# Kernel optimization log

Measured on AMD Instinct MI355X. Metric: run time of the kernel, lower is better.

## Reference

```python
import jax, jax.numpy as jnp
import numpy as np

N, E, H, ED = 20000, 640000, 128, 16


def _lin_init(k, fan_in, fan_out):
    kw, kb = jax.random.split(k)
    lim = 1.0 / np.sqrt(fan_in)
    W = jax.random.uniform(kw, (fan_in, fan_out), jnp.float32, -lim, lim)
    b = jax.random.uniform(kb, (fan_out,), jnp.float32, -lim, lim)
    return W, b


def setup_inputs() -> dict:
    key = jax.random.key(0)
    ks = jax.random.split(key, 12)
    h = jax.random.normal(ks[0], (N, H), jnp.float32)
    x = jax.random.normal(ks[1], (N, 3), jnp.float32)
    edge_index = jax.random.randint(ks[2], (2, E), 0, N, jnp.int32)
    edge_attr = jax.random.normal(ks[3], (E, ED), jnp.float32)
    fixed_mask = jax.random.randint(ks[4], (N,), 0, 2, jnp.int32).astype(bool)
    We1, be1 = _lin_init(ks[5], 2 * H + 1 + ED, H)
    We2, be2 = _lin_init(ks[6], H, H)
    Wx1, bx1 = _lin_init(ks[7], H, H)
    Wx2, bx2 = _lin_init(ks[8], H, 1)
    Wh1, bh1 = _lin_init(ks[9], 2 * H, H)
    Wh2, bh2 = _lin_init(ks[10], H, H)
    return {"h": h, "x": x, "edge_index": edge_index, "edge_attr": edge_attr,
            "fixed_mask": fixed_mask,
            "We1": We1, "be1": be1, "We2": We2, "be2": be2,
            "Wx1": Wx1, "bx1": bx1, "Wx2": Wx2, "bx2": bx2,
            "Wh1": Wh1, "bh1": bh1, "Wh2": Wh2, "bh2": bh2}


def reference(h, x, edge_index, edge_attr, fixed_mask,
              We1, be1, We2, be2, Wx1, bx1, Wx2, bx2, Wh1, bh1, Wh2, bh2):
    src, dst = edge_index[0], edge_index[1]
    n = h.shape[0]
    diff = x[src] - x[dst]                               # [E,3]
    dist_sq_norm = jnp.sum(diff * diff, -1, keepdims=True) / 100.0
    e_in = jnp.concatenate([h[src], h[dst], dist_sq_norm, edge_attr], -1)
    m_ij = jax.nn.silu(jax.nn.silu(e_in @ We1 + be1) @ We2 + be2)  # [E,H]
    coord_w = jnp.tanh(jax.nn.silu(m_ij @ Wx1 + bx1) @ Wx2 + bx2)  # [E,1]
    coord_agg = jax.ops.segment_sum(diff * coord_w, dst, num_segments=n)
    coord_agg = coord_agg * (~fixed_mask).astype(h.dtype)[:, None]
    msg_agg = jax.ops.segment_sum(m_ij, dst, num_segments=n)       # [N,H]
    h_new = h + jax.nn.silu(jnp.concatenate([h, msg_agg], -1) @ Wh1 + bh1) @ Wh2 + bh2
    x_new = x + coord_agg
    return h_new, x_new
```

## Files before the change

kernel.cpp:

```cpp
#include <hip/hip_runtime.h>
#include <hip/hip_bf16.h>
#include <math.h>

#define NN   20000
#define NE   640000
#define HD   128
#define EDIM 16
#define KIN  273
#define P2   136

#define S_PWT   4096
#define S_PWE1M 32768
#define S_PW4   16384
#define S_PWH1  32768
#define S_PWH2  16384

typedef __bf16 bf16x8 __attribute__((ext_vector_type(8)));
typedef float  f32x4  __attribute__((ext_vector_type(4)));

__device__ __forceinline__ float silu_f(float v) {
    const float e = __expf(-v);
    return v * __builtin_amdgcn_rcpf(1.0f + e);
}
__device__ __forceinline__ float tanh_f(float s) {
    const float e = __expf(2.0f * s);
    return 1.0f - 2.0f * __builtin_amdgcn_rcpf(e + 1.0f);
}
__device__ __forceinline__ unsigned short f2bf(float f) {
    __bf16 b = (__bf16)f;
    return __builtin_bit_cast(unsigned short, b);
}
__device__ __forceinline__ float bf2f(unsigned short u) {
    __bf16 b = __builtin_bit_cast(__bf16, u);
    return (float)b;
}
__device__ __forceinline__ unsigned pack2bf(float a, float b) {
    return (unsigned)f2bf(a) | ((unsigned)f2bf(b) << 16);
}

__device__ __forceinline__ void pack_id(const float* __restrict__ W, int Kreal,
                                        unsigned short* __restrict__ P, int idx) {
    const int f = idx >> 9, r = idx & 511;
    const int lane = r >> 3, j = r & 7;
    const int kb = f >> 3, nb = f & 7;
    const int k = kb * 32 + (lane >> 4) * 8 + j;
    const int n = nb * 16 + (lane & 15);
    P[idx] = f2bf((k < Kreal) ? W[(size_t)k * HD + n] : 0.0f);
}
__device__ __forceinline__ void pack_il(const float* __restrict__ W, int Kreal,
                                        unsigned short* __restrict__ P, int idx) {
    const int f = idx >> 9, r = idx & 511;
    const int lane = r >> 3, j = r & 7;
    const int kb = f >> 3, nb = f & 7;
    const int k = kb * 32 + (lane >> 4) * 8 + j;
    const int n = (nb >> 1) * 32 + 2 * (lane & 15) + (nb & 1);
    P[idx] = f2bf((k < Kreal) ? W[(size_t)k * HD + n] : 0.0f);
}

#define ZDW (NN*(HD+3))

__global__ void egnn_prep_kernel(
    const float* __restrict__ h, const int* __restrict__ ei,
    const float* __restrict__ We1, const float* __restrict__ We2,
    const float* __restrict__ Wx1, const float* __restrict__ Wh1,
    const float* __restrict__ Wh2,
    int* __restrict__ zbase,
    unsigned short* __restrict__ hb,
    unsigned short* __restrict__ PWt,  unsigned short* __restrict__ PWe1m,
    unsigned short* __restrict__ PWe2, unsigned short* __restrict__ PWx1,
    unsigned short* __restrict__ PWh1, unsigned short* __restrict__ PWh2,
    int* __restrict__ cnt)
{
    const size_t NH4 = (size_t)NN * HD / 4;
    const size_t Z1 = ZDW, C1 = Z1 + NH4;
    const size_t T1 = C1 + S_PWT, T2 = T1 + S_PWE1M, T3 = T2 + S_PW4;
    const size_t T4 = T3 + S_PW4, T5 = T4 + S_PWH1, T6 = T5 + S_PWH2;
    const size_t TOT = T6 + NE;
    const size_t stride = (size_t)gridDim.x * blockDim.x;
    for (size_t i = (size_t)blockIdx.x * blockDim.x + threadIdx.x; i < TOT; i += stride) {
        if (i < Z1) { zbase[i] = 0; continue; }
        if (i < C1) {
            const size_t r = i - Z1;
            const float4 v = ((const float4*)h)[r];
            unsigned* dst = (unsigned*)&hb[r * 4];
            dst[0] = pack2bf(v.x, v.y);
            dst[1] = pack2bf(v.z, v.w);
            continue;
        }
        if (i < T1) {
            const int idx = (int)(i - C1);
            const int r = idx & 511, nb = idx >> 9;
            const int lane = r >> 3, j = r & 7;
            const int k = 256 + (lane >> 4) * 8 + j;
            const int n = (nb >> 1) * 32 + 2 * (lane & 15) + (nb & 1);
            PWt[idx] = f2bf((k < KIN) ? We1[(size_t)k * HD + n] : 0.0f);
            continue;
        }
        if (i < T2) { pack_il(We1, 256, PWe1m, (int)(i - T1)); continue; }
        if (i < T3) { pack_il(We2, HD, PWe2, (int)(i - T2)); continue; }
        if (i < T4) { pack_il(Wx1, HD, PWx1, (int)(i - T3)); continue; }
        if (i < T5) { pack_id(Wh1, 2 * HD, PWh1, (int)(i - T4)); continue; }
        if (i < T6) { pack_id(Wh2, HD, PWh2, (int)(i - T5)); continue; }
        atomicAdd(&cnt[ei[NE + (i - T6)]], 1);
    }
}

__global__ __launch_bounds__(256, 4) void egnn_pre_kernel(
    const unsigned short* __restrict__ hb,
    const unsigned short* __restrict__ PWe1m, const float* __restrict__ be1,
    const int* __restrict__ cnt, int* __restrict__ cursor,
    unsigned short* __restrict__ preS, unsigned short* __restrict__ preD)
{
    const int t = threadIdx.x;
    if (blockIdx.x == 313) {
        __shared__ int ls[256];
        const int base = t * 79;
        int c[79];
        int s = 0;
        for (int i = 0; i < 79; ++i) {
            const int idx = base + i;
            c[i] = (idx < NN) ? cnt[idx] : 0;
            s += c[i];
        }
        ls[t] = s;
        __syncthreads();
        int v = s;
        for (int off = 1; off < 256; off <<= 1) {
            const int u = (t >= off) ? ls[t - off] : 0;
            __syncthreads();
            v += u;
            ls[t] = v;
            __syncthreads();
        }
        int run = v - s;
        for (int i = 0; i < 79; ++i) {
            const int idx = base + i;
            if (idx < NN) { cursor[idx] = run; run += c[i]; }
        }
        return;
    }
    const int n0 = blockIdx.x * 64;
    const int lane = t & 63, w = t >> 6;
    const int quad = lane >> 4, l16 = lane & 15;
    int arow[4];
    #pragma unroll
    for (int mb = 0; mb < 4; ++mb) arow[mb] = min(n0 + mb * 16 + l16, NN - 1);

    f32x4 accS[4][2], accD[4][2];
    #pragma unroll
    for (int mb = 0; mb < 4; ++mb)
        #pragma unroll
        for (int nt = 0; nt < 2; ++nt) {
            accS[mb][nt] = (f32x4){0.f,0.f,0.f,0.f};
            accD[mb][nt] = (f32x4){0.f,0.f,0.f,0.f};
        }
    #pragma unroll
    for (int kb = 0; kb < 4; ++kb) {
        bf16x8 a[4], bS[2], bD[2];
        #pragma unroll
        for (int mb = 0; mb < 4; ++mb)
            a[mb] = *(const bf16x8*)&hb[(size_t)arow[mb] * HD + kb * 32 + quad * 8];
        #pragma unroll
        for (int nt = 0; nt < 2; ++nt) {
            bS[nt] = *(const bf16x8*)&PWe1m[((kb * 8 + w * 2 + nt) * 64 + lane) * 8];
            bD[nt] = *(const bf16x8*)&PWe1m[(((4 + kb) * 8 + w * 2 + nt) * 64 + lane) * 8];
        }
        #pragma unroll
        for (int mb = 0; mb < 4; ++mb)
            #pragma unroll
            for (int nt = 0; nt < 2; ++nt) {
                accS[mb][nt] = __builtin_amdgcn_mfma_f32_16x16x32_bf16(
                    a[mb], bS[nt], accS[mb][nt], 0, 0, 0);
                accD[mb][nt] = __builtin_amdgcn_mfma_f32_16x16x32_bf16(
                    a[mb], bD[nt], accD[mb][nt], 0, 0, 0);
            }
    }
    const int cb = w * 32 + 2 * l16;
    const float2 b1 = *(const float2*)&be1[cb];
    #pragma unroll
    for (int mb = 0; mb < 4; ++mb)
        #pragma unroll
        for (int r = 0; r < 4; ++r) {
            const int n = n0 + mb * 16 + quad * 4 + r;
            if (n < NN) {
                *(unsigned*)&preS[(size_t)n * HD + cb] =
                    pack2bf(accS[mb][0][r], accS[mb][1][r]);
                *(unsigned*)&preD[(size_t)n * HD + cb] =
                    pack2bf(accD[mb][0][r] + b1.x, accD[mb][1][r] + b1.y);
            }
        }
}

__global__ void egnn_perm_kernel(const int* __restrict__ ei,
                                 int* __restrict__ cursor, int* __restrict__ perm) {
    const int e = blockIdx.x * 256 + threadIdx.x;
    const int pos = atomicAdd(&cursor[ei[NE + e]], 1);
    perm[pos] = e;
}

__global__ __launch_bounds__(256, 6) void egnn_edge_kernel(
    const unsigned short* __restrict__ preS, const unsigned short* __restrict__ preD,
    const float* __restrict__ x,
    const int* __restrict__ ei, const float* __restrict__ eattr,
    const int* __restrict__ perm,
    const unsigned short* __restrict__ PWt,
    const unsigned short* __restrict__ PWe2, const float* __restrict__ be2,
    const unsigned short* __restrict__ PWx1, const float* __restrict__ bx1,
    const float* __restrict__ Wx2, const float* __restrict__ bx2,
    float* __restrict__ msg_agg, float* __restrict__ coord_agg)
{
    __shared__ __align__(16) unsigned short buf[64 * P2];
    __shared__ int   sE[64], sSrc[64], sDst[64];
    __shared__ float sDiff[64][3];
    __shared__ float sW[64];

    const int t  = threadIdx.x;
    const int e0 = blockIdx.x * 64;
    unsigned short* tail = buf;

    if (t < 64) {
        const int e = perm[e0 + t];
        sE[t] = e;
        const int s = ei[e];
        const int d = ei[NE + e];
        sSrc[t] = s; sDst[t] = d;
        const float dx = x[s*3+0] - x[d*3+0];
        const float dy = x[s*3+1] - x[d*3+1];
        const float dz = x[s*3+2] - x[d*3+2];
        sDiff[t][0] = dx; sDiff[t][1] = dy; sDiff[t][2] = dz;
        tail[t * 32 + 0] = f2bf((dx*dx + dy*dy + dz*dz) * 0.01f);
    }
    __syncthreads();

    const int lane = t & 63;
    const int w    = t >> 6;
    const int quad = lane >> 4;
    const int l16  = lane & 15;
    const int cb   = w * 32 + 2 * l16;

    f32x4 preC[4][2];
    #pragma unroll
    for (int mb = 0; mb < 4; ++mb)
        #pragma unroll
        for (int r = 0; r < 4; ++r) {
            const int row = mb * 16 + quad * 4 + r;
            const unsigned us = *(const unsigned*)&preS[(size_t)sSrc[row] * HD + cb];
            const unsigned ud = *(const unsigned*)&preD[(size_t)sDst[row] * HD + cb];
            preC[mb][0][r] = bf2f((unsigned short)(us & 0xffff)) +
                             bf2f((unsigned short)(ud & 0xffff));
            preC[mb][1][r] = bf2f((unsigned short)(us >> 16)) +
                             bf2f((unsigned short)(ud >> 16));
        }

    {
        const int eL = t >> 2, q = t & 3;
        const int eG = sE[eL];
        #pragma unroll
        for (int jj = 0; jj < 8; ++jj) {
            const int col = q * 8 + jj;
            if (col == 0) continue;
            float v = 0.0f;
            if (col <= EDIM) v = eattr[(size_t)eG * EDIM + (col - 1)];
            tail[eL * 32 + col] = f2bf(v);
        }
    }
    __syncthreads();

    f32x4 acc1[4][2];
    {
        bf16x8 a[4], b[2];
        #pragma unroll
        for (int mb = 0; mb < 4; ++mb)
            a[mb] = *(const bf16x8*)&tail[(mb * 16 + l16) * 32 + quad * 8];
        #pragma unroll
        for (int nt = 0; nt < 2; ++nt)
            b[nt] = *(const bf16x8*)&PWt[((w * 2 + nt) * 64 + lane) * 8];
        #pragma unroll
        for (int mb = 0; mb < 4; ++mb)
            #pragma unroll
            for (int nt = 0; nt < 2; ++nt)
                acc1[mb][nt] = __builtin_amdgcn_mfma_f32_16x16x32_bf16(
                    a[mb], b[nt], preC[mb][nt], 0, 0, 0);
    }
    __syncthreads();

    #pragma unroll
    for (int mb = 0; mb < 4; ++mb)
        #pragma unroll
        for (int r = 0; r < 4; ++r) {
            const int row = mb * 16 + quad * 4 + r;
            *(unsigned*)&buf[row * P2 + cb] =
                pack2bf(silu_f(acc1[mb][0][r]), silu_f(acc1[mb][1][r]));
        }
    __syncthreads();

    f32x4 acc2[4][2];
    #pragma unroll
    for (int mb = 0; mb < 4; ++mb)
        #pragma unroll
        for (int nt = 0; nt < 2; ++nt) acc2[mb][nt] = (f32x4){0.f,0.f,0.f,0.f};
    #pragma unroll
    for (int kb = 0; kb < 4; ++kb) {
        bf16x8 a[4], b[2];
        #pragma unroll
        for (int mb = 0; mb < 4; ++mb)
            a[mb] = *(const bf16x8*)&buf[(mb * 16 + l16) * P2 + kb * 32 + quad * 8];
        #pragma unroll
        for (int nt = 0; nt < 2; ++nt)
            b[nt] = *(const bf16x8*)&PWe2[((kb * 8 + w * 2 + nt) * 64 + lane) * 8];
        #pragma unroll
        for (int mb = 0; mb < 4; ++mb)
            #pragma unroll
            for (int nt = 0; nt < 2; ++nt)
                acc2[mb][nt] = __builtin_amdgcn_mfma_f32_16x16x32_bf16(
                    a[mb], b[nt], acc2[mb][nt], 0, 0, 0);
    }
    __syncthreads();

    {
        const float2 b2 = *(const float2*)&be2[cb];
        #pragma unroll
        for (int mb = 0; mb < 4; ++mb)
            #pragma unroll
            for (int r = 0; r < 4; ++r) {
                const int row = mb * 16 + quad * 4 + r;
                *(unsigned*)&buf[row * P2 + cb] =
                    pack2bf(silu_f(acc2[mb][0][r] + b2.x),
                            silu_f(acc2[mb][1][r] + b2.y));
            }
    }
    __syncthreads();

    {
        const int cp = t & 63;
        const int r0 = (t >> 6) * 16;
        float a0 = 0.0f, a1 = 0.0f;
        #pragma unroll 4
        for (int r = 0; r < 16; ++r) {
            const int row = r0 + r;
            const int d   = sDst[row];
            const unsigned u = *(const unsigned*)&buf[row * P2 + 2 * cp];
            a0 += bf2f((unsigned short)(u & 0xffff));
            a1 += bf2f((unsigned short)(u >> 16));
            const bool flush = (r == 15) || (sDst[row + 1] != d);
            if (flush) {
                atomicAdd(&msg_agg[(size_t)d * HD + 2 * cp], a0);
                atomicAdd(&msg_agg[(size_t)d * HD + 2 * cp + 1], a1);
                a0 = 0.0f; a1 = 0.0f;
            }
        }
    }

    f32x4 acc3[4][2];
    #pragma unroll
    for (int mb = 0; mb < 4; ++mb)
        #pragma unroll
        for (int nt = 0; nt < 2; ++nt) acc3[mb][nt] = (f32x4){0.f,0.f,0.f,0.f};
    #pragma unroll
    for (int kb = 0; kb < 4; ++kb) {
        bf16x8 a[4], b[2];
        #pragma unroll
        for (int mb = 0; mb < 4; ++mb)
            a[mb] = *(const bf16x8*)&buf[(mb * 16 + l16) * P2 + kb * 32 + quad * 8];
        #pragma unroll
        for (int nt = 0; nt < 2; ++nt)
            b[nt] = *(const bf16x8*)&PWx1[((kb * 8 + w * 2 + nt) * 64 + lane) * 8];
        #pragma unroll
        for (int mb = 0; mb < 4; ++mb)
            #pragma unroll
            for (int nt = 0; nt < 2; ++nt)
                acc3[mb][nt] = __builtin_amdgcn_mfma_f32_16x16x32_bf16(
                    a[mb], b[nt], acc3[mb][nt], 0, 0, 0);
    }
    float p[4][4];
    {
        const float2 bx = *(const float2*)&bx1[cb];
        const float2 w2 = *(const float2*)&Wx2[cb];
        #pragma unroll
        for (int mb = 0; mb < 4; ++mb)
            #pragma unroll
            for (int r = 0; r < 4; ++r)
                p[mb][r] = silu_f(acc3[mb][0][r] + bx.x) * w2.x +
                           silu_f(acc3[mb][1][r] + bx.y) * w2.y;
        #pragma unroll
        for (int off = 8; off >= 1; off >>= 1)
            #pragma unroll
            for (int mb = 0; mb < 4; ++mb)
                #pragma unroll
                for (int r = 0; r < 4; ++r)
                    p[mb][r] += __shfl_xor(p[mb][r], off, 64);
    }
    __syncthreads();

    if (l16 == 0) {
        float* red = reinterpret_cast<float*>(buf);
        #pragma unroll
        for (int mb = 0; mb < 4; ++mb)
            #pragma unroll
            for (int r = 0; r < 4; ++r)
                red[w * 64 + mb * 16 + quad * 4 + r] = p[mb][r];
    }
    __syncthreads();
    if (t < 64) {
        const float* red = reinterpret_cast<const float*>(buf);
        sW[t] = tanh_f(red[t] + red[64 + t] + red[128 + t] + red[192 + t] + bx2[0]);
    }
    __syncthreads();

    if (w < 3) {
        const int dstv = sDst[lane];
        float v = sDiff[lane][w] * sW[lane];
        #pragma unroll
        for (int off = 1; off <= 32; off <<= 1) {
            const int   dn = __shfl_down(dstv, off, 64);
            const float vn = __shfl_down(v, off, 64);
            if (lane + off < 64 && dn == dstv) v += vn;
        }
        const int up = __shfl_up(dstv, 1, 64);
        if (lane == 0 || up != dstv)
            atomicAdd(&coord_agg[(size_t)dstv * 3 + w], v);
    }
}

__global__ __launch_bounds__(256, 4) void egnn_node_kernel(
    const unsigned short* __restrict__ hb, const float* __restrict__ h,
    const float* __restrict__ x, const int* __restrict__ fixed_mask,
    const unsigned short* __restrict__ PWh1, const float* __restrict__ bh1,
    const unsigned short* __restrict__ PWh2, const float* __restrict__ bh2,
    const float* __restrict__ msg_agg, const float* __restrict__ coord_agg,
    float* __restrict__ out_h, float* __restrict__ out_x)
{
    __shared__ __align__(16) unsigned short sTn[64 * P2];
    const int t  = threadIdx.x;
    const int n0 = blockIdx.x * 64;
    const int lane = t & 63, w = t >> 6;
    const int quad = lane >> 4, l16 = lane & 15;

    if (t < 192) {
        const int ln = t / 3, d3 = t - ln * 3;
        const int n  = n0 + ln;
        if (n < NN) {
            const float add = (fixed_mask[n] != 0) ? 0.0f : coord_agg[(size_t)n*3 + d3];
            out_x[(size_t)n*3 + d3] = x[(size_t)n*3 + d3] + add;
        }
    }

    int nrow[4];
    #pragma unroll
    for (int mb = 0; mb < 4; ++mb) nrow[mb] = min(n0 + mb * 16 + l16, NN - 1);

    f32x4 acc[4][2];
    #pragma unroll
    for (int mb = 0; mb < 4; ++mb)
        #pragma unroll
        for (int nt = 0; nt < 2; ++nt) acc[mb][nt] = (f32x4){0.f,0.f,0.f,0.f};

    #pragma unroll
    for (int kb = 0; kb < 8; ++kb) {
        bf16x8 a[4], b[2];
        if (kb < 4) {
            #pragma unroll
            for (int mb = 0; mb < 4; ++mb)
                a[mb] = *(const bf16x8*)&hb[(size_t)nrow[mb] * HD + kb * 32 + quad * 8];
        } else {
            #pragma unroll
            for (int mb = 0; mb < 4; ++mb) {
                const float* mp = msg_agg + (size_t)nrow[mb] * HD + (kb - 4) * 32 + quad * 8;
                const float4 v0 = ((const float4*)mp)[0];
                const float4 v1 = ((const float4*)mp)[1];
                bf16x8 av;
                av[0]=(__bf16)v0.x; av[1]=(__bf16)v0.y; av[2]=(__bf16)v0.z; av[3]=(__bf16)v0.w;
                av[4]=(__bf16)v1.x; av[5]=(__bf16)v1.y; av[6]=(__bf16)v1.z; av[7]=(__bf16)v1.w;
                a[mb] = av;
            }
        }
        #pragma unroll
        for (int nt = 0; nt < 2; ++nt)
            b[nt] = *(const bf16x8*)&PWh1[((kb * 8 + w * 2 + nt) * 64 + lane) * 8];
        #pragma unroll
        for (int mb = 0; mb < 4; ++mb)
            #pragma unroll
            for (int nt = 0; nt < 2; ++nt)
                acc[mb][nt] = __builtin_amdgcn_mfma_f32_16x16x32_bf16(
                    a[mb], b[nt], acc[mb][nt], 0, 0, 0);
    }
    #pragma unroll
    for (int nt = 0; nt < 2; ++nt) {
        const int col = w * 32 + nt * 16 + l16;
        const float bias = bh1[col];
        #pragma unroll
        for (int mb = 0; mb < 4; ++mb)
            #pragma unroll
            for (int r = 0; r < 4; ++r) {
                const int row = mb * 16 + quad * 4 + r;
                sTn[row * P2 + col] = f2bf(silu_f(acc[mb][nt][r] + bias));
            }
    }
    __syncthreads();

    #pragma unroll
    for (int mb = 0; mb < 4; ++mb)
        #pragma unroll
        for (int nt = 0; nt < 2; ++nt) acc[mb][nt] = (f32x4){0.f,0.f,0.f,0.f};
    #pragma unroll
    for (int kb = 0; kb < 4; ++kb) {
        bf16x8 a[4], b[2];
        #pragma unroll
        for (int mb = 0; mb < 4; ++mb)
            a[mb] = *(const bf16x8*)&sTn[(mb * 16 + l16) * P2 + kb * 32 + quad * 8];
        #pragma unroll
        for (int nt = 0; nt < 2; ++nt)
            b[nt] = *(const bf16x8*)&PWh2[((kb * 8 + w * 2 + nt) * 64 + lane) * 8];
        #pragma unroll
        for (int mb = 0; mb < 4; ++mb)
            #pragma unroll
            for (int nt = 0; nt < 2; ++nt)
                acc[mb][nt] = __builtin_amdgcn_mfma_f32_16x16x32_bf16(
                    a[mb], b[nt], acc[mb][nt], 0, 0, 0);
    }
    #pragma unroll
    for (int nt = 0; nt < 2; ++nt) {
        const int col = w * 32 + nt * 16 + l16;
        const float bias = bh2[col];
        #pragma unroll
        for (int mb = 0; mb < 4; ++mb)
            #pragma unroll
            for (int r = 0; r < 4; ++r) {
                const int row = mb * 16 + quad * 4 + r;
                const int n   = n0 + row;
                if (n < NN)
                    out_h[(size_t)n * HD + col] =
                        h[(size_t)n * HD + col] + acc[mb][nt][r] + bias;
            }
    }
}

extern "C" void kernel_launch(void* const* d_in, const int* in_sizes, int n_in,
                              void* d_out, int out_size, void* d_ws, size_t ws_size,
                              hipStream_t stream)
{
    const float* h     = (const float*)d_in[0];
    const float* x     = (const float*)d_in[1];
    const int*   ei    = (const int*)d_in[2];
    const float* eattr = (const float*)d_in[3];
    const int*   fmask = (const int*)d_in[4];
    const float* We1   = (const float*)d_in[5];
    const float* be1   = (const float*)d_in[6];
    const float* We2   = (const float*)d_in[7];
    const float* be2   = (const float*)d_in[8];
    const float* Wx1   = (const float*)d_in[9];
    const float* bx1   = (const float*)d_in[10];
    const float* Wx2   = (const float*)d_in[11];
    const float* bx2   = (const float*)d_in[12];
    const float* Wh1   = (const float*)d_in[13];
    const float* bh1   = (const float*)d_in[14];
    const float* Wh2   = (const float*)d_in[15];
    const float* bh2   = (const float*)d_in[16];

    float* msg    = (float*)d_ws;
    float* coord  = msg + (size_t)NN * HD;
    int*   cnt    = (int*)(coord + (size_t)NN * 3);
    int*   cursor = cnt + NN;
    int*   perm   = cursor + NN;
    unsigned short* hb    = (unsigned short*)(perm + NE);
    unsigned short* preS  = hb + (size_t)NN * HD;
    unsigned short* preD  = preS + (size_t)NN * HD;
    unsigned short* PWt   = preD + (size_t)NN * HD;
    unsigned short* PWe1m = PWt + S_PWT;
    unsigned short* PWe2  = PWe1m + S_PWE1M;
    unsigned short* PWx1  = PWe2 + S_PW4;
    unsigned short* PWh1  = PWx1 + S_PW4;
    unsigned short* PWh2  = PWh1 + S_PWH1;

    float* out_h = (float*)d_out;
    float* out_x = out_h + (size_t)NN * HD;

    hipMemsetAsync(cnt, 0, (size_t)NN * sizeof(int), stream);
    egnn_prep_kernel<<<1024, 256, 0, stream>>>(
        h, ei, We1, We2, Wx1, Wh1, Wh2, (int*)d_ws,
        hb, PWt, PWe1m, PWe2, PWx1, PWh1, PWh2, cnt);
    egnn_pre_kernel<<<314, 256, 0, stream>>>(hb, PWe1m, be1, cnt, cursor, preS, preD);
    egnn_perm_kernel<<<NE / 256, 256, 0, stream>>>(ei, cursor, perm);
    egnn_edge_kernel<<<NE / 64, 256, 0, stream>>>(
        preS, preD, x, ei, eattr, perm, PWt, PWe2, be2, PWx1, bx1,
        Wx2, bx2, msg, coord);
    egnn_node_kernel<<<(NN + 63) / 64, 256, 0, stream>>>(
        hb, h, x, fmask, PWh1, bh1, PWh2, bh2, msg, coord, out_h, out_x);
}
```

Before: 379.5 us.

## Split edge MLP MFMA work by rows per wave with interleaved weight packing

Each wave now owns 16 edge rows across all 128 output columns, where before it owned 32 columns across all 64 rows. Weights are repacked so each lane holds 8 contiguous columns, which enables 16-byte gathers of preS/preD and uint4 stores to LDS. It also removes the cross-wave LDS reduction and one barrier in the coord-weight head. In exchange each wave now loads all B fragments (8 per k-block) instead of 2, which shifts traffic from A-fragment LDS reads to weight reads.

```diff
diff --git a/kernel.cpp b/kernel.cpp
--- a/kernel.cpp
+++ b/kernel.cpp
@@ -37,6 +37,8 @@
 __device__ __forceinline__ unsigned pack2bf(float a, float b) {
     return (unsigned)f2bf(a) | ((unsigned)f2bf(b) << 16);
 }
+__device__ __forceinline__ float lo16(unsigned u) { return bf2f((unsigned short)(u & 0xffff)); }
+__device__ __forceinline__ float hi16(unsigned u) { return bf2f((unsigned short)(u >> 16)); }
 
 __device__ __forceinline__ void pack_id(const float* __restrict__ W, int Kreal,
                                         unsigned short* __restrict__ P, int idx) {
@@ -54,6 +56,15 @@
     const int kb = f >> 3, nb = f & 7;
     const int k = kb * 32 + (lane >> 4) * 8 + j;
     const int n = (nb >> 1) * 32 + 2 * (lane & 15) + (nb & 1);
+    P[idx] = f2bf((k < Kreal) ? W[(size_t)k * HD + n] : 0.0f);
+}
+__device__ __forceinline__ void pack_i8(const float* __restrict__ W, int Kreal,
+                                        unsigned short* __restrict__ P, int idx) {
+    const int f = idx >> 9, r = idx & 511;
+    const int lane = r >> 3, j = r & 7;
+    const int kb = f >> 3, nb = f & 7;
+    const int k = kb * 32 + (lane >> 4) * 8 + j;
+    const int n = 8 * (lane & 15) + nb;
     P[idx] = f2bf((k < Kreal) ? W[(size_t)k * HD + n] : 0.0f);
 }
 
@@ -92,13 +103,13 @@
             const int r = idx & 511, nb = idx >> 9;
             const int lane = r >> 3, j = r & 7;
             const int k = 256 + (lane >> 4) * 8 + j;
-            const int n = (nb >> 1) * 32 + 2 * (lane & 15) + (nb & 1);
+            const int n = 8 * (lane & 15) + nb;
             PWt[idx] = f2bf((k < KIN) ? We1[(size_t)k * HD + n] : 0.0f);
             continue;
         }
         if (i < T2) { pack_il(We1, 256, PWe1m, (int)(i - T1)); continue; }
-        if (i < T3) { pack_il(We2, HD, PWe2, (int)(i - T2)); continue; }
-        if (i < T4) { pack_il(Wx1, HD, PWx1, (int)(i - T3)); continue; }
+        if (i < T3) { pack_i8(We2, HD, PWe2, (int)(i - T2)); continue; }
+        if (i < T4) { pack_i8(Wx1, HD, PWx1, (int)(i - T3)); continue; }
         if (i < T5) { pack_id(Wh1, 2 * HD, PWh1, (int)(i - T4)); continue; }
         if (i < T6) { pack_id(Wh2, HD, PWh2, (int)(i - T5)); continue; }
         atomicAdd(&cnt[ei[NE + (i - T6)]], 1);
@@ -236,21 +247,22 @@
     const int w    = t >> 6;
     const int quad = lane >> 4;
     const int l16  = lane & 15;
-    const int cb   = w * 32 + 2 * l16;
-
-    f32x4 preC[4][2];
-    #pragma unroll
-    for (int mb = 0; mb < 4; ++mb)
-        #pragma unroll
-        for (int r = 0; r < 4; ++r) {
-            const int row = mb * 16 + quad * 4 + r;
-            const unsigned us = *(const unsigned*)&preS[(size_t)sSrc[row] * HD + cb];
-            const unsigned ud = *(const unsigned*)&preD[(size_t)sDst[row] * HD + cb];
-            preC[mb][0][r] = bf2f((unsigned short)(us & 0xffff)) +
-                             bf2f((unsigned short)(ud & 0xffff));
-            preC[mb][1][r] = bf2f((unsigned short)(us >> 16)) +
-                             bf2f((unsigned short)(ud >> 16));
-        }
+    const int c8   = 8 * l16;
+    int rowg[4];
+    #pragma unroll
+    for (int r = 0; r < 4; ++r) rowg[r] = w * 16 + quad * 4 + r;
+
+    f32x4 acc[8];
+    #pragma unroll
+    for (int r = 0; r < 4; ++r) {
+        const int row = rowg[r];
+        const uint4 us = *(const uint4*)&preS[(size_t)sSrc[row] * HD + c8];
+        const uint4 ud = *(const uint4*)&preD[(size_t)sDst[row] * HD + c8];
+        acc[0][r] = lo16(us.x) + lo16(ud.x);  acc[1][r] = hi16(us.x) + hi16(ud.x);
+        acc[2][r] = lo16(us.y) + lo16(ud.y);  acc[3][r] = hi16(us.y) + hi16(ud.y);
+        acc[4][r] = lo16(us.z) + lo16(ud.z);  acc[5][r] = hi16(us.z) + hi16(ud.z);
+        acc[6][r] = lo16(us.w) + lo16(ud.w);  acc[7][r] = hi16(us.w) + hi16(ud.w);
+    }
 
     {
         const int eL = t >> 2, q = t & 3;
@@ -266,68 +278,52 @@
     }
     __syncthreads();
 
-    f32x4 acc1[4][2];
     {
-        bf16x8 a[4], b[2];
-        #pragma unroll
-        for (int mb = 0; mb < 4; ++mb)
-            a[mb] = *(const bf16x8*)&tail[(mb * 16 + l16) * 32 + quad * 8];
-        #pragma unroll
-        for (int nt = 0; nt < 2; ++nt)
-            b[nt] = *(const bf16x8*)&PWt[((w * 2 + nt) * 64 + lane) * 8];
-        #pragma unroll
-        for (int mb = 0; mb < 4; ++mb)
-            #pragma unroll
-            for (int nt = 0; nt < 2; ++nt)
-                acc1[mb][nt] = __builtin_amdgcn_mfma_f32_16x16x32_bf16(
-                    a[mb], b[nt], preC[mb][nt], 0, 0, 0);
-    }
-    __syncthreads();
-
-    #pragma unroll
-    for (int mb = 0; mb < 4; ++mb)
+        const bf16x8 a = *(const bf16x8*)&tail[(w * 16 + l16) * 32 + quad * 8];
+        #pragma unroll
+        for (int nt = 0; nt < 8; ++nt) {
+            const bf16x8 b = *(const bf16x8*)&PWt[(nt * 64 + lane) * 8];
+            acc[nt] = __builtin_amdgcn_mfma_f32_16x16x32_bf16(a, b, acc[nt], 0, 0, 0);
+        }
+    }
+    __syncthreads();
+
+    #pragma unroll
+    for (int r = 0; r < 4; ++r) {
+        uint4 o;
+        o.x = pack2bf(silu_f(acc[0][r]), silu_f(acc[1][r]));
+        o.y = pack2bf(silu_f(acc[2][r]), silu_f(acc[3][r]));
+        o.z = pack2bf(silu_f(acc[4][r]), silu_f(acc[5][r]));
+        o.w = pack2bf(silu_f(acc[6][r]), silu_f(acc[7][r]));
+        *(uint4*)&buf[rowg[r] * P2 + c8] = o;
+    }
+    __syncthreads();
+
+    #pragma unroll
+    for (int nt = 0; nt < 8; ++nt) acc[nt] = (f32x4){0.f,0.f,0.f,0.f};
+    #pragma unroll
+    for (int kb = 0; kb < 4; ++kb) {
+        const bf16x8 a = *(const bf16x8*)&buf[(w * 16 + l16) * P2 + kb * 32 + quad * 8];
+        #pragma unroll
+        for (int nt = 0; nt < 8; ++nt) {
+            const bf16x8 b = *(const bf16x8*)&PWe2[((kb * 8 + nt) * 64 + lane) * 8];
+            acc[nt] = __builtin_amdgcn_mfma_f32_16x16x32_bf16(a, b, acc[nt], 0, 0, 0);
+        }
+    }
+    __syncthreads();
+
+    {
+        const float4 ba = *(const float4*)&be2[c8];
+        const float4 bb = *(const float4*)&be2[c8 + 4];
         #pragma unroll
         for (int r = 0; r < 4; ++r) {
-            const int row = mb * 16 + quad * 4 + r;
-            *(unsigned*)&buf[row * P2 + cb] =
-                pack2bf(silu_f(acc1[mb][0][r]), silu_f(acc1[mb][1][r]));
-        }
-    __syncthreads();
-
-    f32x4 acc2[4][2];
-    #pragma unroll
-    for (int mb = 0; mb < 4; ++mb)
-        #pragma unroll
-        for (int nt = 0; nt < 2; ++nt) acc2[mb][nt] = (f32x4){0.f,0.f,0.f,0.f};
-    #pragma unroll
-    for (int kb = 0; kb < 4; ++kb) {
-        bf16x8 a[4], b[2];
-        #pragma unroll
-        for (int mb = 0; mb < 4; ++mb)
-            a[mb] = *(const bf16x8*)&buf[(mb * 16 + l16) * P2 + kb * 32 + quad * 8];
-        #pragma unroll
-        for (int nt = 0; nt < 2; ++nt)
-            b[nt] = *(const bf16x8*)&PWe2[((kb * 8 + w * 2 + nt) * 64 + lane) * 8];
-        #pragma unroll
-        for (int mb = 0; mb < 4; ++mb)
-            #pragma unroll
-            for (int nt = 0; nt < 2; ++nt)
-                acc2[mb][nt] = __builtin_amdgcn_mfma_f32_16x16x32_bf16(
-                    a[mb], b[nt], acc2[mb][nt], 0, 0, 0);
-    }
-    __syncthreads();
-
-    {
-        const float2 b2 = *(const float2*)&be2[cb];
-        #pragma unroll
-        for (int mb = 0; mb < 4; ++mb)
-            #pragma unroll
-            for (int r = 0; r < 4; ++r) {
-                const int row = mb * 16 + quad * 4 + r;
-                *(unsigned*)&buf[row * P2 + cb] =
-                    pack2bf(silu_f(acc2[mb][0][r] + b2.x),
-                            silu_f(acc2[mb][1][r] + b2.y));
-            }
+            uint4 o;
+            o.x = pack2bf(silu_f(acc[0][r] + ba.x), silu_f(acc[1][r] + ba.y));
+            o.y = pack2bf(silu_f(acc[2][r] + ba.z), silu_f(acc[3][r] + ba.w));
+            o.z = pack2bf(silu_f(acc[4][r] + bb.x), silu_f(acc[5][r] + bb.y));
+            o.w = pack2bf(silu_f(acc[6][r] + bb.z), silu_f(acc[7][r] + bb.w));
+            *(uint4*)&buf[rowg[r] * P2 + c8] = o;
+        }
     }
     __syncthreads();
 
@@ -340,8 +336,8 @@
             const int row = r0 + r;
             const int d   = sDst[row];
             const unsigned u = *(const unsigned*)&buf[row * P2 + 2 * cp];
-            a0 += bf2f((unsigned short)(u & 0xffff));
-            a1 += bf2f((unsigned short)(u >> 16));
+            a0 += lo16(u);
+            a1 += hi16(u);
             const bool flush = (r == 15) || (sDst[row + 1] != d);
             if (flush) {
                 atomicAdd(&msg_agg[(size_t)d * HD + 2 * cp], a0);
@@ -351,59 +347,40 @@
         }
     }
 
-    f32x4 acc3[4][2];
-    #pragma unroll
-    for (int mb = 0; mb < 4; ++mb)
-        #pragma unroll
-        for (int nt = 0; nt < 2; ++nt) acc3[mb][nt] = (f32x4){0.f,0.f,0.f,0.f};
+    #pragma unroll
+    for (int nt = 0; nt < 8; ++nt) acc[nt] = (f32x4){0.f,0.f,0.f,0.f};
     #pragma unroll
     for (int kb = 0; kb < 4; ++kb) {
-        bf16x8 a[4], b[2];
-        #pragma unroll
-        for (int mb = 0; mb < 4; ++mb)
-            a[mb] = *(const bf16x8*)&buf[(mb * 16 + l16) * P2 + kb * 32 + quad * 8];
-        #pragma unroll
-        for (int nt = 0; nt < 2; ++nt)
-            b[nt] = *(const bf16x8*)&PWx1[((kb * 8 + w * 2 + nt) * 64 + lane) * 8];
-        #pragma unroll
-        for (int mb = 0; mb < 4; ++mb)
-            #pragma unroll
-            for (int nt = 0; nt < 2; ++nt)
-                acc3[mb][nt] = __builtin_amdgcn_mfma_f32_16x16x32_bf16(
-                    a[mb], b[nt], acc3[mb][nt], 0, 0, 0);
-    }
-    float p[4][4];
+        const bf16x8 a = *(const bf16x8*)&buf[(w * 16 + l16) * P2 + kb * 32 + quad * 8];
+        #pragma unroll
+        for (int nt = 0; nt < 8; ++nt) {
+            const bf16x8 b = *(const bf16x8*)&PWx1[((kb * 8 + nt) * 64 + lane) * 8];
+            acc[nt] = __builtin_amdgcn_mfma_f32_16x16x32_bf16(a, b, acc[nt], 0, 0, 0);
+        }
+    }
     {
-        const float2 bx = *(const float2*)&bx1[cb];
-        const float2 w2 = *(const float2*)&Wx2[cb];
-        #pragma unroll
-        for (int mb = 0; mb < 4; ++mb)
+        const float4 ba = *(const float4*)&bx1[c8];
+        const float4 bb = *(const float4*)&bx1[c8 + 4];
+        const float4 wa = *(const float4*)&Wx2[c8];
+        const float4 wb = *(const float4*)&Wx2[c8 + 4];
+        float p[4];
+        #pragma unroll
+        for (int r = 0; r < 4; ++r) {
+            p[r] = silu_f(acc[0][r] + ba.x) * wa.x + silu_f(acc[1][r] + ba.y) * wa.y
+                 + silu_f(acc[2][r] + ba.z) * wa.z + silu_f(acc[3][r] + ba.w) * wa.w
+                 + silu_f(acc[4][r] + bb.x) * wb.x + silu_f(acc[5][r] + bb.y) * wb.y
+                 + silu_f(acc[6][r] + bb.z) * wb.z + silu_f(acc[7][r] + bb.w) * wb.w;
+        }
+        #pragma unroll
+        for (int off = 8; off >= 1; off >>= 1)
             #pragma unroll
             for (int r = 0; r < 4; ++r)
-                p[mb][r] = silu_f(acc3[mb][0][r] + bx.x) * w2.x +
-                           silu_f(acc3[mb][1][r] + bx.y) * w2.y;
-        #pragma unroll
-        for (int off = 8; off >= 1; off >>= 1)
-            #pragma unroll
-            for (int mb = 0; mb < 4; ++mb)
-                #pragma unroll
-                for (int r = 0; r < 4; ++r)
-                    p[mb][r] += __shfl_xor(p[mb][r], off, 64);
-    }
-    __syncthreads();
-
-    if (l16 == 0) {
-        float* red = reinterpret_cast<float*>(buf);
-        #pragma unroll
-        for (int mb = 0; mb < 4; ++mb)
+                p[r] += __shfl_xor(p[r], off, 64);
+        if (l16 == 0) {
             #pragma unroll
             for (int r = 0; r < 4; ++r)
-                red[w * 64 + mb * 16 + quad * 4 + r] = p[mb][r];
-    }
-    __syncthreads();
-    if (t < 64) {
-        const float* red = reinterpret_cast<const float*>(buf);
-        sW[t] = tanh_f(red[t] + red[64 + t] + red[128 + t] + red[192 + t] + bx2[0]);
+                sW[rowg[r]] = tanh_f(p[r] + bx2[0]);
+        }
     }
     __syncthreads();
 
```

After: 496.4 us. 1.31x slower.
